# Performance work log

Hardware: AMD Instinct MI355X
Metric: run time of the kernel (lower is better)

Reference implementation:

```python
import jax, jax.numpy as jnp
import numpy as np
import math

T, B, E, H, NEXP = 512, 8, 1024, 32, 256
DH = E // H
S = T + NEXP
SCALING = (DH / 1) ** 0.5 / DH  # = 1/sqrt(head_dim) for d_tilde=1
LN_EPS = 1e-5


def _xavier(key, shape, gain):
    fan_in, fan_out = shape[1], shape[0]
    a = gain * math.sqrt(6.0 / (fan_in + fan_out))
    return jax.random.uniform(key, shape, jnp.float32, -a, a)


def setup_inputs() -> dict:
    key = jax.random.key(0)
    ks = jax.random.split(key, 12)
    g = 1.0 / math.sqrt(2.0)  # xavier gain 1/sqrt(2*d_tilde)
    return {
        "query": jax.random.normal(ks[0], (T, B, E), jnp.float32),
        "attn_bias": jax.random.normal(ks[1], (B * H, T, S), jnp.float32) * 0.1,
        "outcell_index": jax.random.randint(ks[2], (B, NEXP), 0, T - 1),
        "expand_mask": jax.random.randint(ks[3], (B, NEXP), 0, 2).astype(bool),
        "key_padding_mask": jnp.zeros((B, T), bool),
        "Wq": _xavier(ks[4], (E, E), g),
        "bq": jnp.zeros((E,), jnp.float32),
        "Wk": _xavier(ks[5], (E, E), g),  # k_proj has no bias (k_bias=False)
        "Wv": _xavier(ks[6], (E, E), g),
        "bv": jnp.zeros((E,), jnp.float32),
        "Wo": _xavier(ks[7], (E, E), 1.0),
        "bo": jnp.zeros((E,), jnp.float32),
        "ln_g": jnp.ones((E,), jnp.float32),
        "ln_b": jnp.zeros((E,), jnp.float32),
    }


def reference(query, attn_bias, outcell_index, expand_mask, key_padding_mask,
              Wq, bq, Wk, Wv, bv, Wo, bo, ln_g, ln_b):
    # projections (Time x Batch x Channel)
    q = (query @ Wq.T + bq) * SCALING          # [T,B,E]
    k = query @ Wk.T                            # [T,B,E] (no bias)
    v = query @ Wv.T + bv                       # [T,B,E]

    # PBC gather-expansion of K/V along time dim (note +1 offset as in source)
    idx = outcell_index.T + 1                   # [NEXP,B]
    idx3 = jnp.broadcast_to(idx[:, :, None], (NEXP, B, E))
    expand_k = jnp.take_along_axis(k, idx3, axis=0)
    expand_v = jnp.take_along_axis(v, idx3, axis=0)
    k = jnp.concatenate([k, expand_k], axis=0)  # [S,B,E]
    v = jnp.concatenate([v, expand_v], axis=0)  # [S,B,E]

    # split heads
    qh = q.reshape(T, B, H, DH)
    kh = k.reshape(S, B, H, DH)
    vh = v.reshape(S, B, H, DH)

    scores = jnp.einsum("tbhd,sbhd->bhts", qh, kh)  # [B,H,T,S]
    scores = scores + attn_bias.reshape(B, H, T, S)

    mask = jnp.concatenate([key_padding_mask, expand_mask], axis=1)  # [B,S]
    scores = jnp.where(mask[:, None, None, :], -jnp.inf, scores)

    probs = jax.nn.softmax(scores, axis=-1)      # [B,H,T,S]

    attn = jnp.einsum("bhts,sbhd->tbhd", probs, vh).reshape(T, B, E)

    # layer norm then output projection
    mu = attn.mean(-1, keepdims=True)
    var = ((attn - mu) ** 2).mean(-1, keepdims=True)
    attn = (attn - mu) * jax.lax.rsqrt(var + LN_EPS) * ln_g + ln_b
    out = attn @ Wo.T + bo                       # [T,B,E]

    attn_weights_mean = probs.mean(axis=1)       # [B,T,S] (mean over heads)
    return out, attn_weights_mean
```

## Files before the change

### kernel.cpp

```cpp
#include <hip/hip_runtime.h>

#define DEV __device__ __forceinline__

typedef short bh8 __attribute__((ext_vector_type(8)));
typedef short bh4 __attribute__((ext_vector_type(4)));
typedef float fx4 __attribute__((ext_vector_type(4)));

#define T_ 512
#define B_ 8
#define E_ 1024
#define H_ 32
#define DH_ 32
#define S_ 768
#define NEXP_ 256
#define SCALING_ 0.17677669529663687f
#define OFF_QB    ((size_t)0)
#define OFF_WB    ((size_t)8388608)
#define OFF_QRM   ((size_t)16777216)
#define OFF_KRM   ((size_t)25165824)
#define OFF_VRM   ((size_t)33554432)
#define OFF_KBF   ((size_t)41943040)
#define OFF_VT    ((size_t)54525952)
#define OFF_ATTN  ((size_t)67108864)
#define OFF_XHAT  ((size_t)75497472)
#define OFF_MASK  ((size_t)83886080)
#define OFF_FLAG  ((size_t)83910656)

#define BARRIER_LGKM() do { \
  asm volatile("s_waitcnt lgkmcnt(0)" ::: "memory"); \
  __builtin_amdgcn_s_barrier(); \
} while (0)

#define WAIT_VM0_BARRIER() do { \
  asm volatile("s_waitcnt vmcnt(0)" ::: "memory"); \
  __builtin_amdgcn_s_barrier(); \
} while (0)

DEV float bf2f(short u) {
  union { unsigned int i; float f; } x;
  x.i = ((unsigned int)(unsigned short)u) << 16;
  return x.f;
}
DEV short f2bf(float f) {
  union { float f; unsigned int u; } x; x.f = f;
  unsigned int r = x.u + 0x7fffu + ((x.u >> 16) & 1u);
  return (short)(r >> 16);
}
DEV void gl_lds16(const void* g, void* l) {
  __builtin_amdgcn_global_load_lds(
      (const __attribute__((address_space(1))) unsigned int*)g,
      (__attribute__((address_space(3))) unsigned int*)l, 16, 0, 0);
}

__global__ __launch_bounds__(256) void conv_all(
    const float* __restrict__ q, const float* __restrict__ wq,
    const float* __restrict__ wk, const float* __restrict__ wv,
    const float* __restrict__ wo, short* __restrict__ QB, short* __restrict__ WB) {
  size_t i4 = ((size_t)blockIdx.x * 256 + threadIdx.x) * 4;
  const float* s; short* d;
  if (i4 < (size_t)4194304) { s = q + i4; d = QB + i4; }
  else {
    size_t r = i4 - 4194304; int m = (int)(r >> 20); size_t o = r & 1048575;
    const float* ws4[4] = {wq, wk, wv, wo};
    s = ws4[m] + o; d = WB + ((size_t)m << 20) + o;
  }
  fx4 v = *(const fx4*)s;
  bh4 p = { f2bf(v[0]), f2bf(v[1]), f2bf(v[2]), f2bf(v[3]) };
  *(bh4*)d = p;
}

__global__ void detect_bool(const unsigned char* __restrict__ em, int* __restrict__ flag) {
  __shared__ int f;
  if (threadIdx.x == 0) f = 0;
  __syncthreads();
  for (int i = threadIdx.x; i < 2048; i += 256)
    if ((i & 3) && em[i]) atomicOr(&f, 1);
  __syncthreads();
  if (threadIdx.x == 0) *flag = f;
}

__global__ __launch_bounds__(256) void qkv_gemm(
    const short* __restrict__ QB, const short* __restrict__ WB,
    const float* __restrict__ bq, const float* __restrict__ bv,
    short* __restrict__ q_rm, short* __restrict__ k_rm, short* __restrict__ v_rm) {
  __shared__ __align__(16) short As[128 * 32];
  __shared__ __align__(16) short Ws[128 * 32];
  const int tid = threadIdx.x;
  const int mt = blockIdx.x, nt = blockIdx.y;
  const int mat = nt >> 3;
  const size_t m0 = (size_t)mt * 128;
  const int n0 = (nt & 7) << 7;
  const short* W = WB + (size_t)mat * (1024 * 1024);
  const int l = tid & 63, wv_ = tid >> 6;
  const int lt = l & 15, g = l >> 4;
  const int wm = wv_ >> 1, wn = wv_ & 1;
  fx4 acc[4][4];
#pragma unroll
  for (int i = 0; i < 4; ++i)
#pragma unroll
    for (int j = 0; j < 4; ++j) acc[i][j] = fx4{0.f, 0.f, 0.f, 0.f};

  const int r0 = tid >> 2, c0 = tid & 3;
  for (int kt = 0; kt < 32; ++kt) {
    const int k0 = kt * 32;
    __syncthreads();
    gl_lds16(QB + (m0 + r0) * 1024 + k0 + c0 * 8,        As + r0 * 32 + c0 * 8);
    gl_lds16(QB + (m0 + 64 + r0) * 1024 + k0 + c0 * 8,   As + (64 + r0) * 32 + c0 * 8);
    gl_lds16(W + (size_t)(n0 + r0) * 1024 + k0 + c0 * 8,      Ws + r0 * 32 + c0 * 8);
    gl_lds16(W + (size_t)(n0 + 64 + r0) * 1024 + k0 + c0 * 8, Ws + (64 + r0) * 32 + c0 * 8);
    __syncthreads();
    bh8 af[4], wf[4];
#pragma unroll
    for (int i = 0; i < 4; ++i) af[i] = *(const bh8*)(As + (wm * 64 + i * 16 + lt) * 32 + g * 8);
#pragma unroll
    for (int j = 0; j < 4; ++j) wf[j] = *(const bh8*)(Ws + (wn * 64 + j * 16 + lt) * 32 + g * 8);
#pragma unroll
    for (int i = 0; i < 4; ++i)
#pragma unroll
      for (int j = 0; j < 4; ++j)
        acc[i][j] = __builtin_amdgcn_mfma_f32_16x16x32_bf16(af[i], wf[j], acc[i][j], 0, 0, 0);
  }
  short* outp = (mat == 0) ? q_rm : (mat == 1) ? k_rm : v_rm;
#pragma unroll
  for (int i = 0; i < 4; ++i) {
    const size_t rowb = m0 + wm * 64 + i * 16 + g * 4;
#pragma unroll
    for (int j = 0; j < 4; ++j) {
      const int col = n0 + wn * 64 + j * 16 + lt;
      const float bias = (mat == 0) ? bq[col] : (mat == 2) ? bv[col] : 0.0f;
#pragma unroll
      for (int jj = 0; jj < 4; ++jj) {
        float v = acc[i][j][jj] + bias;
        if (mat == 0) v *= SCALING_;
        outp[(rowb + jj) * 1024 + col] = f2bf(v);
      }
    }
  }
}

__global__ __launch_bounds__(256) void repack(
    const short* __restrict__ k_rm, const short* __restrict__ v_rm,
    const int* __restrict__ oc, const unsigned char* __restrict__ em,
    const unsigned char* __restrict__ kp, const int* __restrict__ flag,
    short* __restrict__ kbf, short* __restrict__ vT, float* __restrict__ maskval) {
  __shared__ __align__(16) short lv[64 * 40];
  const int bid = blockIdx.x, tid = threadIdx.x;
  if (bid < 3072) {
    int u = bid * 256 + tid;
    int d8 = u & 3;
    int s = (u >> 2) % 768;
    int hb = (u >> 2) / 768;
    int b = hb >> 5, h = hb & 31;
    int srct = (s < 512) ? s : (oc[b * 256 + (s - 512)] + 1);
    bh8 val = *(const bh8*)(k_rm + ((size_t)srct * 8 + b) * 1024 + h * 32 + d8 * 8);
    *(bh8*)(kbf + ((size_t)hb * 768 + s) * 32 + d8 * 8) = val;
  } else if (bid < 6144) {
    int idx = bid - 3072;
    int c = idx % 12;
    int hb = idx / 12;
    int b = hb >> 5, h = hb & 31;
    int s_loc = tid >> 2, d8 = tid & 3;
    int s = c * 64 + s_loc;
    int srct = (s < 512) ? s : (oc[b * 256 + (s - 512)] + 1);
    bh8 val = *(const bh8*)(v_rm + ((size_t)srct * 8 + b) * 1024 + h * 32 + d8 * 8);
    *(bh8*)(lv + s_loc * 40 + d8 * 8) = val;
    __syncthreads();
    int d = tid >> 3, sj = tid & 7;
    bh8 o;
#pragma unroll
    for (int k = 0; k < 8; ++k) o[k] = lv[(sj * 8 + k) * 40 + d];
    *(bh8*)(vT + ((size_t)hb * 32 + d) * 768 + c * 64 + sj * 8) = o;
  } else {
    int u = (bid - 6144) * 256 + tid;
    if (u < 6144) {
      int s = u % 768, b = u / 768;
      int m;
      if (*flag) {
        m = (s < 512) ? (int)kp[b * 512 + s] : (int)em[b * 256 + (s - 512)];
      } else {
        const int* kpi = (const int*)kp; const int* emi = (const int*)em;
        m = (s < 512) ? kpi[b * 512 + s] : emi[b * 256 + (s - 512)];
      }
      maskval[u] = m ? -3.0e38f : 0.0f;
    }
  }
}

__global__ __launch_bounds__(512) void attn_kernel(
    const short* __restrict__ q_rm, const short* __restrict__ kbf,
    const short* __restrict__ vT, const float* __restrict__ bias,
    const float* __restrict__ maskval, short* __restrict__ attn_bf,
    float* __restrict__ mean_out) {
  __shared__ __align__(16) float bias_lds[2][16 * 768];
  __shared__ __align__(16) short p_st[8 * 16 * 40];
  __shared__ float lpart[8][16];
  __shared__ __align__(16) float attred[2][8 * 64 * 8];
  __shared__ __align__(16) float maskv[768];

  const int tid = threadIdx.x, blk = blockIdx.x;
  const int tt = blk & 31, b = blk >> 5;
  const int t0 = tt * 16;
  const int w = tid >> 6, l = tid & 63, lt = l & 15, g = l >> 4;
  const int sbase = w * 96;

  for (int u = tid; u < 768; u += 512) maskv[u] = maskval[b * 768 + u];

  const float* bias_base = bias + ((size_t)(b * 32) * 512 + t0) * 768;
#pragma unroll
  for (int r = 0; r < 6; ++r)
    gl_lds16(bias_base + (size_t)(r * 512 + tid) * 4,
             (char*)bias_lds[0] + (size_t)(r * 512 + tid) * 16);
  asm volatile("s_waitcnt lgkmcnt(0) vmcnt(0)" ::: "memory");
  __builtin_amdgcn_s_barrier();

  const fx4 zf = {0.f, 0.f, 0.f, 0.f};
  float msum[24];
#pragma unroll
  for (int i = 0; i < 24; ++i) msum[i] = 0.f;

  for (int hh = 0; hh < 32; ++hh) {
    const int cur = hh & 1;
    const int bh = b * 32 + hh;

    if (hh < 31) {
      const float* nb = bias_base + (size_t)(hh + 1) * 512 * 768;
#pragma unroll
      for (int r = 0; r < 6; ++r)
        gl_lds16(nb + (size_t)(r * 512 + tid) * 4,
                 (char*)bias_lds[cur ^ 1] + (size_t)(r * 512 + tid) * 16);
    }

    const bh8 qf = *(const bh8*)(q_rm + ((size_t)(t0 + lt) * 8 + b) * 1024 + hh * 32 + g * 8);
    const short* kp_ = kbf + (size_t)bh * 768 * 32;

    unsigned exu[12];
    float ls0 = 0.f, ls1 = 0.f, ls2 = 0.f, ls3 = 0.f;
#pragma unroll
    for (int c = 0; c < 6; ++c) {
      const int s0 = sbase + c * 16;
      bh8 kf = *(const bh8*)(kp_ + (s0 + lt) * 32 + g * 8);
      fx4 sc = __builtin_amdgcn_mfma_f32_16x16x32_bf16(qf, kf, zf, 0, 0, 0);
      const float mv = maskv[s0 + lt];
      const float* bl = bias_lds[cur] + (g * 4) * 768 + s0 + lt;
      float e0 = __expf(sc[0] + bl[0]       + mv);
      float e1 = __expf(sc[1] + bl[768]     + mv);
      float e2 = __expf(sc[2] + bl[2 * 768] + mv);
      float e3 = __expf(sc[3] + bl[3 * 768] + mv);
      ls0 += e0; ls1 += e1; ls2 += e2; ls3 += e3;
      exu[c * 2]     = (unsigned)(unsigned short)f2bf(e0) | ((unsigned)(unsigned short)f2bf(e1) << 16);
      exu[c * 2 + 1] = (unsigned)(unsigned short)f2bf(e2) | ((unsigned)(unsigned short)f2bf(e3) << 16);
    }
#pragma unroll
    for (int m = 1; m < 16; m <<= 1) {
      ls0 += __shfl_xor(ls0, m); ls1 += __shfl_xor(ls1, m);
      ls2 += __shfl_xor(ls2, m); ls3 += __shfl_xor(ls3, m);
    }
    if (lt == 0) {
      lpart[w][g * 4 + 0] = ls0; lpart[w][g * 4 + 1] = ls1;
      lpart[w][g * 4 + 2] = ls2; lpart[w][g * 4 + 3] = ls3;
    }
    BARRIER_LGKM();
    float linv[4];
#pragma unroll
    for (int jj = 0; jj < 4; ++jj) {
      float s8v = 0.f;
#pragma unroll
      for (int w2 = 0; w2 < 8; ++w2) s8v += lpart[w2][g * 4 + jj];
      linv[jj] = 1.0f / s8v;
    }
    float sacc = 0.f;
#pragma unroll
    for (int w2 = 0; w2 < 8; ++w2) sacc += lpart[w2][lt];
    const float linv_acc = 1.0f / sacc;

    fx4 acc0 = zf, acc1 = zf;
    const short* vp0 = vT + ((size_t)bh * 32 + lt) * 768;
    const short* vp1 = vp0 + 16 * 768;
    short* pw_base = p_st + w * 640;
#pragma unroll
    for (int c2 = 0; c2 < 3; ++c2) {
      const int s0 = sbase + c2 * 32;
#pragma unroll
      for (int cc = 0; cc < 2; ++cc) {
        const int c = c2 * 2 + cc;
        unsigned u01 = exu[c * 2], u23 = exu[c * 2 + 1];
        short* pcol = pw_base + cc * 16 + lt;
        pcol[(g * 4 + 0) * 40] = (short)(u01 & 0xffffu);
        pcol[(g * 4 + 1) * 40] = (short)(u01 >> 16);
        pcol[(g * 4 + 2) * 40] = (short)(u23 & 0xffffu);
        pcol[(g * 4 + 3) * 40] = (short)(u23 >> 16);
        msum[c * 4 + 0] += bf2f((short)(u01 & 0xffffu)) * linv[0];
        msum[c * 4 + 1] += bf2f((short)(u01 >> 16)) * linv[1];
        msum[c * 4 + 2] += bf2f((short)(u23 & 0xffffu)) * linv[2];
        msum[c * 4 + 3] += bf2f((short)(u23 >> 16)) * linv[3];
      }
      bh8 pf = *(const bh8*)(pw_base + lt * 40 + g * 8);
      bh8 vf0 = *(const bh8*)(vp0 + s0 + g * 8);
      bh8 vf1 = *(const bh8*)(vp1 + s0 + g * 8);
      acc0 = __builtin_amdgcn_mfma_f32_16x16x32_bf16(vf0, pf, acc0, 0, 0, 0);
      acc1 = __builtin_amdgcn_mfma_f32_16x16x32_bf16(vf1, pf, acc1, 0, 0, 0);
    }
#pragma unroll
    for (int jj = 0; jj < 4; ++jj) { acc0[jj] *= linv_acc; acc1[jj] *= linv_acc; }

    float* ar = attred[cur] + (w * 64 + l) * 8;
    *(fx4*)(ar) = acc0;
    *(fx4*)(ar + 4) = acc1;
    BARRIER_LGKM();
    if (w < 2) {
      const float* ab = attred[cur];
      float s0v = 0.f, s1v = 0.f, s2v = 0.f, s3v = 0.f;
#pragma unroll
      for (int w2 = 0; w2 < 8; ++w2) {
        const float* a2 = ab + (w2 * 64 + l) * 8 + w * 4;
        s0v += a2[0]; s1v += a2[1]; s2v += a2[2]; s3v += a2[3];
      }
      bh4 o = { f2bf(s0v), f2bf(s1v), f2bf(s2v), f2bf(s3v) };
      *(bh4*)(attn_bf + ((size_t)(t0 + lt) * 8 + b) * 1024 + hh * 32 + w * 16 + g * 4) = o;
    }
    WAIT_VM0_BARRIER();
  }

  float* mob = mean_out + ((size_t)b * 512 + t0) * 768;
#pragma unroll
  for (int c = 0; c < 6; ++c) {
    const int s = sbase + c * 16 + lt;
#pragma unroll
    for (int jj = 0; jj < 4; ++jj) {
      mob[(size_t)(g * 4 + jj) * 768 + s] = msum[c * 4 + jj] * 0.03125f;
    }
  }
}

__global__ __launch_bounds__(256) void ln_kernel(
    const short* __restrict__ attn_bf, const float* __restrict__ lg,
    const float* __restrict__ lb, short* __restrict__ xhat) {
  const int w = threadIdx.x >> 6, l = threadIdx.x & 63;
  const size_t row = (size_t)blockIdx.x * 4 + w;
  const short* x = attn_bf + row * 1024 + l * 16;
  bh8 a0 = *(const bh8*)x, a1 = *(const bh8*)(x + 8);
  float xs[16];
#pragma unroll
  for (int i = 0; i < 8; ++i) { xs[i] = bf2f(a0[i]); xs[8 + i] = bf2f(a1[i]); }
  float s1 = 0.f, s2 = 0.f;
#pragma unroll
  for (int i = 0; i < 16; ++i) { s1 += xs[i]; s2 += xs[i] * xs[i]; }
  for (int m = 1; m < 64; m <<= 1) { s1 += __shfl_xor(s1, m); s2 += __shfl_xor(s2, m); }
  const float mu = s1 * (1.0f / 1024.0f);
  float var = s2 * (1.0f / 1024.0f) - mu * mu;
  var = fmaxf(var, 0.f);
  const float rs = rsqrtf(var + 1e-5f);
  const float* lgp = lg + l * 16;
  const float* lbp = lb + l * 16;
  bh8 o0, o1;
#pragma unroll
  for (int i = 0; i < 8; ++i) {
    o0[i] = f2bf((xs[i] - mu) * rs * lgp[i] + lbp[i]);
    o1[i] = f2bf((xs[8 + i] - mu) * rs * lgp[8 + i] + lbp[8 + i]);
  }
  short* y = xhat + row * 1024 + l * 16;
  *(bh8*)y = o0;
  *(bh8*)(y + 8) = o1;
}

__global__ __launch_bounds__(256) void out_gemm(
    const short* __restrict__ XH, const short* __restrict__ WoB,
    const float* __restrict__ bo, float* __restrict__ out) {
  __shared__ __align__(16) short As[128 * 32];
  __shared__ __align__(16) short Ws[128 * 32];
  const int tid = threadIdx.x;
  const int mt = blockIdx.x, nt = blockIdx.y;
  const size_t m0 = (size_t)mt * 128;
  const int n0 = nt << 7;
  const int l = tid & 63, wv_ = tid >> 6;
  const int lt = l & 15, g = l >> 4;
  const int wm = wv_ >> 1, wn = wv_ & 1;
  fx4 acc[4][4];
#pragma unroll
  for (int i = 0; i < 4; ++i)
#pragma unroll
    for (int j = 0; j < 4; ++j) acc[i][j] = fx4{0.f, 0.f, 0.f, 0.f};
  const int r0 = tid >> 2, c0 = tid & 3;
  for (int kt = 0; kt < 32; ++kt) {
    const int k0 = kt * 32;
    __syncthreads();
    gl_lds16(XH + (m0 + r0) * 1024 + k0 + c0 * 8,        As + r0 * 32 + c0 * 8);
    gl_lds16(XH + (m0 + 64 + r0) * 1024 + k0 + c0 * 8,   As + (64 + r0) * 32 + c0 * 8);
    gl_lds16(WoB + (size_t)(n0 + r0) * 1024 + k0 + c0 * 8,      Ws + r0 * 32 + c0 * 8);
    gl_lds16(WoB + (size_t)(n0 + 64 + r0) * 1024 + k0 + c0 * 8, Ws + (64 + r0) * 32 + c0 * 8);
    __syncthreads();
    bh8 af[4], wf[4];
#pragma unroll
    for (int i = 0; i < 4; ++i) af[i] = *(const bh8*)(As + (wm * 64 + i * 16 + lt) * 32 + g * 8);
#pragma unroll
    for (int j = 0; j < 4; ++j) wf[j] = *(const bh8*)(Ws + (wn * 64 + j * 16 + lt) * 32 + g * 8);
#pragma unroll
    for (int i = 0; i < 4; ++i)
#pragma unroll
      for (int j = 0; j < 4; ++j)
        acc[i][j] = __builtin_amdgcn_mfma_f32_16x16x32_bf16(af[i], wf[j], acc[i][j], 0, 0, 0);
  }
#pragma unroll
  for (int i = 0; i < 4; ++i) {
    const size_t rowb = m0 + wm * 64 + i * 16 + g * 4;
#pragma unroll
    for (int j = 0; j < 4; ++j) {
      const int col = n0 + wn * 64 + j * 16 + lt;
      const float bb = bo[col];
#pragma unroll
      for (int jj = 0; jj < 4; ++jj)
        out[(rowb + jj) * 1024 + col] = acc[i][j][jj] + bb;
    }
  }
}

extern "C" void kernel_launch(void* const* d_in, const int* in_sizes, int n_in,
                              void* d_out, int out_size, void* d_ws, size_t ws_size,
                              hipStream_t stream) {
  const float* query = (const float*)d_in[0];
  const float* attn_bias = (const float*)d_in[1];
  const int* oc = (const int*)d_in[2];
  const unsigned char* em = (const unsigned char*)d_in[3];
  const unsigned char* kp = (const unsigned char*)d_in[4];
  const float* Wq = (const float*)d_in[5];
  const float* bq = (const float*)d_in[6];
  const float* Wk = (const float*)d_in[7];
  const float* Wv = (const float*)d_in[8];
  const float* bv = (const float*)d_in[9];
  const float* Wo = (const float*)d_in[10];
  const float* bo = (const float*)d_in[11];
  const float* lg = (const float*)d_in[12];
  const float* lb = (const float*)d_in[13];

  char* w = (char*)d_ws;
  short* QB    = (short*)(w + OFF_QB);
  short* WB    = (short*)(w + OFF_WB);
  short* QRM   = (short*)(w + OFF_QRM);
  short* KRM   = (short*)(w + OFF_KRM);
  short* VRM   = (short*)(w + OFF_VRM);
  short* KBF   = (short*)(w + OFF_KBF);
  short* VT    = (short*)(w + OFF_VT);
  short* ATTN  = (short*)(w + OFF_ATTN);
  short* XHAT  = (short*)(w + OFF_XHAT);
  float* MASK  = (float*)(w + OFF_MASK);
  int*   FLAG  = (int*)(w + OFF_FLAG);

  float* out0 = (float*)d_out;
  float* mean_out = out0 + (size_t)T_ * B_ * E_;

  conv_all<<<8192, 256, 0, stream>>>(query, Wq, Wk, Wv, Wo, QB, WB);
  detect_bool<<<1, 256, 0, stream>>>(em, FLAG);
  qkv_gemm<<<dim3(32, 24), 256, 0, stream>>>(QB, WB, bq, bv, QRM, KRM, VRM);
  repack<<<6168, 256, 0, stream>>>(KRM, VRM, oc, em, kp, FLAG, KBF, VT, MASK);
  attn_kernel<<<256, 512, 0, stream>>>(QRM, KBF, VT, attn_bias, MASK, ATTN, mean_out);
  ln_kernel<<<1024, 256, 0, stream>>>(ATTN, lg, lb, XHAT);
  out_gemm<<<dim3(32, 8), 256, 0, stream>>>(XHAT, WB + (size_t)3 * 1024 * 1024, bo, out0);
}
```

Before: 290.3 us.

## Fuse layernorm into attention tail, fold flag detect into conversion, coarsen repack

Removes the separate layernorm kernel by having each attention block normalize its own 16 output rows after the head loop, reading back the bf16 rows it just wrote. The bool-detection kernel is merged into block 0 of the conversion kernel. The repack kernel now processes 4 K chunks or 2 V chunks per block, cutting the grid size. This aims to cut launch overhead and tail inefficiency, but relies on intra-block visibility of global writes before the fused layernorm reads them.

```diff
diff --git a/kernel.cpp b/kernel.cpp
--- a/kernel.cpp
+++ b/kernel.cpp
@@ -55,7 +55,17 @@
 __global__ __launch_bounds__(256) void conv_all(
     const float* __restrict__ q, const float* __restrict__ wq,
     const float* __restrict__ wk, const float* __restrict__ wv,
-    const float* __restrict__ wo, short* __restrict__ QB, short* __restrict__ WB) {
+    const float* __restrict__ wo, short* __restrict__ QB, short* __restrict__ WB,
+    const unsigned char* __restrict__ em, int* __restrict__ flag) {
+  if (blockIdx.x == 0) {
+    __shared__ int f;
+    if (threadIdx.x == 0) f = 0;
+    __syncthreads();
+    for (int i = threadIdx.x; i < 2048; i += 256)
+      if ((i & 3) && em[i]) atomicOr(&f, 1);
+    __syncthreads();
+    if (threadIdx.x == 0) *flag = f;
+  }
   size_t i4 = ((size_t)blockIdx.x * 256 + threadIdx.x) * 4;
   const float* s; short* d;
   if (i4 < (size_t)4194304) { s = q + i4; d = QB + i4; }
@@ -67,16 +77,6 @@
   fx4 v = *(const fx4*)s;
   bh4 p = { f2bf(v[0]), f2bf(v[1]), f2bf(v[2]), f2bf(v[3]) };
   *(bh4*)d = p;
-}
-
-__global__ void detect_bool(const unsigned char* __restrict__ em, int* __restrict__ flag) {
-  __shared__ int f;
-  if (threadIdx.x == 0) f = 0;
-  __syncthreads();
-  for (int i = threadIdx.x; i < 2048; i += 256)
-    if ((i & 3) && em[i]) atomicOr(&f, 1);
-  __syncthreads();
-  if (threadIdx.x == 0) *flag = f;
 }
 
 __global__ __launch_bounds__(256) void qkv_gemm(
@@ -143,35 +143,46 @@
     const int* __restrict__ oc, const unsigned char* __restrict__ em,
     const unsigned char* __restrict__ kp, const int* __restrict__ flag,
     short* __restrict__ kbf, short* __restrict__ vT, float* __restrict__ maskval) {
-  __shared__ __align__(16) short lv[64 * 40];
+  __shared__ __align__(16) short lv[2][64 * 40];
   const int bid = blockIdx.x, tid = threadIdx.x;
-  if (bid < 3072) {
-    int u = bid * 256 + tid;
-    int d8 = u & 3;
-    int s = (u >> 2) % 768;
-    int hb = (u >> 2) / 768;
-    int b = hb >> 5, h = hb & 31;
-    int srct = (s < 512) ? s : (oc[b * 256 + (s - 512)] + 1);
-    bh8 val = *(const bh8*)(k_rm + ((size_t)srct * 8 + b) * 1024 + h * 32 + d8 * 8);
-    *(bh8*)(kbf + ((size_t)hb * 768 + s) * 32 + d8 * 8) = val;
-  } else if (bid < 6144) {
-    int idx = bid - 3072;
-    int c = idx % 12;
-    int hb = idx / 12;
-    int b = hb >> 5, h = hb & 31;
+  if (bid < 768) {
+#pragma unroll
+    for (int k = 0; k < 4; ++k) {
+      int u = bid * 1024 + k * 256 + tid;
+      int d8 = u & 3;
+      int s = (u >> 2) % 768;
+      int hb = (u >> 2) / 768;
+      int b = hb >> 5, h = hb & 31;
+      int srct = (s < 512) ? s : (oc[b * 256 + (s - 512)] + 1);
+      bh8 val = *(const bh8*)(k_rm + ((size_t)srct * 8 + b) * 1024 + h * 32 + d8 * 8);
+      *(bh8*)(kbf + ((size_t)hb * 768 + s) * 32 + d8 * 8) = val;
+    }
+  } else if (bid < 2304) {
+    int idx2 = bid - 768;
     int s_loc = tid >> 2, d8 = tid & 3;
-    int s = c * 64 + s_loc;
-    int srct = (s < 512) ? s : (oc[b * 256 + (s - 512)] + 1);
-    bh8 val = *(const bh8*)(v_rm + ((size_t)srct * 8 + b) * 1024 + h * 32 + d8 * 8);
-    *(bh8*)(lv + s_loc * 40 + d8 * 8) = val;
+#pragma unroll
+    for (int k = 0; k < 2; ++k) {
+      int chunk = idx2 * 2 + k;
+      int c = chunk % 12, hb = chunk / 12;
+      int b = hb >> 5, h = hb & 31;
+      int s = c * 64 + s_loc;
+      int srct = (s < 512) ? s : (oc[b * 256 + (s - 512)] + 1);
+      bh8 val = *(const bh8*)(v_rm + ((size_t)srct * 8 + b) * 1024 + h * 32 + d8 * 8);
+      *(bh8*)(lv[k] + s_loc * 40 + d8 * 8) = val;
+    }
     __syncthreads();
     int d = tid >> 3, sj = tid & 7;
-    bh8 o;
-#pragma unroll
-    for (int k = 0; k < 8; ++k) o[k] = lv[(sj * 8 + k) * 40 + d];
-    *(bh8*)(vT + ((size_t)hb * 32 + d) * 768 + c * 64 + sj * 8) = o;
+#pragma unroll
+    for (int k = 0; k < 2; ++k) {
+      int chunk = idx2 * 2 + k;
+      int c = chunk % 12, hb = chunk / 12;
+      bh8 o;
+#pragma unroll
+      for (int e = 0; e < 8; ++e) o[e] = lv[k][(sj * 8 + e) * 40 + d];
+      *(bh8*)(vT + ((size_t)hb * 32 + d) * 768 + c * 64 + sj * 8) = o;
+    }
   } else {
-    int u = (bid - 6144) * 256 + tid;
+    int u = (bid - 2304) * 256 + tid;
     if (u < 6144) {
       int s = u % 768, b = u / 768;
       int m;
@@ -190,7 +201,8 @@
     const short* __restrict__ q_rm, const short* __restrict__ kbf,
     const short* __restrict__ vT, const float* __restrict__ bias,
     const float* __restrict__ maskval, short* __restrict__ attn_bf,
-    float* __restrict__ mean_out) {
+    float* __restrict__ mean_out, const float* __restrict__ lg,
+    const float* __restrict__ lb, short* __restrict__ xhat) {
   __shared__ __align__(16) float bias_lds[2][16 * 768];
   __shared__ __align__(16) short p_st[8 * 16 * 40];
   __shared__ float lpart[8][16];
@@ -321,6 +333,36 @@
     WAIT_VM0_BARRIER();
   }
 
+#pragma unroll
+  for (int r2 = 0; r2 < 2; ++r2) {
+    const int trow = t0 + w * 2 + r2;
+    const size_t row = (size_t)trow * 8 + b;
+    const short* x = attn_bf + row * 1024 + l * 16;
+    bh8 a0 = *(const bh8*)x, a1 = *(const bh8*)(x + 8);
+    float xs[16];
+#pragma unroll
+    for (int i = 0; i < 8; ++i) { xs[i] = bf2f(a0[i]); xs[8 + i] = bf2f(a1[i]); }
+    float s1 = 0.f, s2 = 0.f;
+#pragma unroll
+    for (int i = 0; i < 16; ++i) { s1 += xs[i]; s2 += xs[i] * xs[i]; }
+    for (int m = 1; m < 64; m <<= 1) { s1 += __shfl_xor(s1, m); s2 += __shfl_xor(s2, m); }
+    const float mu = s1 * (1.0f / 1024.0f);
+    float var = s2 * (1.0f / 1024.0f) - mu * mu;
+    var = fmaxf(var, 0.f);
+    const float rs = rsqrtf(var + 1e-5f);
+    const float* lgp = lg + l * 16;
+    const float* lbp = lb + l * 16;
+    bh8 o0, o1;
+#pragma unroll
+    for (int i = 0; i < 8; ++i) {
+      o0[i] = f2bf((xs[i] - mu) * rs * lgp[i] + lbp[i]);
+      o1[i] = f2bf((xs[8 + i] - mu) * rs * lgp[8 + i] + lbp[8 + i]);
+    }
+    short* y = xhat + row * 1024 + l * 16;
+    *(bh8*)y = o0;
+    *(bh8*)(y + 8) = o1;
+  }
+
   float* mob = mean_out + ((size_t)b * 512 + t0) * 768;
 #pragma unroll
   for (int c = 0; c < 6; ++c) {
@@ -330,37 +372,6 @@
       mob[(size_t)(g * 4 + jj) * 768 + s] = msum[c * 4 + jj] * 0.03125f;
     }
   }
-}
-
-__global__ __launch_bounds__(256) void ln_kernel(
-    const short* __restrict__ attn_bf, const float* __restrict__ lg,
-    const float* __restrict__ lb, short* __restrict__ xhat) {
-  const int w = threadIdx.x >> 6, l = threadIdx.x & 63;
-  const size_t row = (size_t)blockIdx.x * 4 + w;
-  const short* x = attn_bf + row * 1024 + l * 16;
-  bh8 a0 = *(const bh8*)x, a1 = *(const bh8*)(x + 8);
-  float xs[16];
-#pragma unroll
-  for (int i = 0; i < 8; ++i) { xs[i] = bf2f(a0[i]); xs[8 + i] = bf2f(a1[i]); }
-  float s1 = 0.f, s2 = 0.f;
-#pragma unroll
-  for (int i = 0; i < 16; ++i) { s1 += xs[i]; s2 += xs[i] * xs[i]; }
-  for (int m = 1; m < 64; m <<= 1) { s1 += __shfl_xor(s1, m); s2 += __shfl_xor(s2, m); }
-  const float mu = s1 * (1.0f / 1024.0f);
-  float var = s2 * (1.0f / 1024.0f) - mu * mu;
-  var = fmaxf(var, 0.f);
-  const float rs = rsqrtf(var + 1e-5f);
-  const float* lgp = lg + l * 16;
-  const float* lbp = lb + l * 16;
-  bh8 o0, o1;
-#pragma unroll
-  for (int i = 0; i < 8; ++i) {
-    o0[i] = f2bf((xs[i] - mu) * rs * lgp[i] + lbp[i]);
-    o1[i] = f2bf((xs[8 + i] - mu) * rs * lgp[8 + i] + lbp[8 + i]);
-  }
-  short* y = xhat + row * 1024 + l * 16;
-  *(bh8*)y = o0;
-  *(bh8*)(y + 8) = o1;
 }
 
 __global__ __launch_bounds__(256) void out_gemm(
@@ -448,11 +459,10 @@
   float* out0 = (float*)d_out;
   float* mean_out = out0 + (size_t)T_ * B_ * E_;
 
-  conv_all<<<8192, 256, 0, stream>>>(query, Wq, Wk, Wv, Wo, QB, WB);
-  detect_bool<<<1, 256, 0, stream>>>(em, FLAG);
+  conv_all<<<8192, 256, 0, stream>>>(query, Wq, Wk, Wv, Wo, QB, WB, em, FLAG);
   qkv_gemm<<<dim3(32, 24), 256, 0, stream>>>(QB, WB, bq, bv, QRM, KRM, VRM);
-  repack<<<6168, 256, 0, stream>>>(KRM, VRM, oc, em, kp, FLAG, KBF, VT, MASK);
-  attn_kernel<<<256, 512, 0, stream>>>(QRM, KBF, VT, attn_bias, MASK, ATTN, mean_out);
-  ln_kernel<<<1024, 256, 0, stream>>>(ATTN, lg, lb, XHAT);
+  repack<<<2328, 256, 0, stream>>>(KRM, VRM, oc, em, kp, FLAG, KBF, VT, MASK);
+  attn_kernel<<<256, 512, 0, stream>>>(QRM, KBF, VT, attn_bias, MASK, ATTN,
+                                       mean_out, lg, lb, XHAT);
   out_gemm<<<dim3(32, 8), 256, 0, stream>>>(XHAT, WB + (size_t)3 * 1024 * 1024, bo, out0);
 }
```

Measured after the change: 262.7 us. -9.5%, faster.
